# Performance work log

Measured on AMD Instinct MI355X. Metric: run time of the kernel, lower is better.

The kernel has to match this reference:

```python
import jax, jax.numpy as jnp
import numpy as np

RC = 5.0  # cosine cutoff radius

def ssp(z):
    # shifted softplus, SchNet activation
    return jax.nn.softplus(z) - jnp.log(2.0).astype(z.dtype)

def setup_inputs():
    key = jax.random.key(0)
    ks = jax.random.split(key, 16)
    B, Na, Nn, G, F = 2, 2048, 48, 50, 128
    e = jax.random.normal(ks[0], (B, Na, 1), jnp.float32)
    x = jax.random.normal(ks[1], (B, Na, F), jnp.float32)
    t = jax.random.normal(ks[2], (B, Na, 1), jnp.float32)
    r_ij = jax.random.uniform(ks[3], (B, Na, Nn), jnp.float32) * 6.0  # some beyond cutoff
    neighbors = jax.random.randint(ks[4], (B, Na, Nn), 0, Na)
    pairwise_mask = jax.random.randint(ks[5], (B, Na, Nn), 0, 2).astype(jnp.int32)
    f_ij = jax.random.normal(ks[6], (B, Na, Nn, G), jnp.float32)
    def lin(k, fan_in, fan_out):
        return jax.random.normal(k, (fan_in, fan_out), jnp.float32) / np.sqrt(fan_in).astype(np.float32)
    Wf1 = lin(ks[7], G, F); bf1 = jnp.zeros((F,), jnp.float32)
    Wf2 = lin(ks[8], F, F); bf2 = jnp.zeros((F,), jnp.float32)
    Wq = lin(ks[9], F, F)
    Wk = lin(ks[10], F, F)
    Wv = lin(ks[11], F, F)
    Wo = lin(ks[12], F, F); bo = jnp.zeros((F,), jnp.float32)
    return dict(e=e, x=x, t=t, r_ij=r_ij, neighbors=neighbors, pairwise_mask=pairwise_mask,
                f_ij=f_ij, Wf1=Wf1, bf1=bf1, Wf2=Wf2, bf2=bf2, Wq=Wq, Wk=Wk, Wv=Wv, Wo=Wo, bo=bo)

def reference(e, x, t, r_ij, neighbors, pairwise_mask, f_ij,
              Wf1, bf1, Wf2, bf2, Wq, Wk, Wv, Wo, bo):
    B, Na, Nn = neighbors.shape
    F = x.shape[-1]
    # continuous filter from expanded distances: W = filter_network(2*f_ij - 1)
    W = 2.0 * f_ij - 1.0
    W = ssp(W @ Wf1 + bf1) @ Wf2 + bf2                # [B,Na,Nn,F]
    # cosine cutoff
    C = (0.5 * (jnp.cos(jnp.pi * r_ij / RC) + 1.0) * (r_ij < RC))[..., None]  # [B,Na,Nn,1]
    W = W * C
    # gather neighbor embeddings: y[b,i,n,:] = x[b, neighbors[b,i,n], :]
    idx = neighbors.reshape(B, Na * Nn)
    y = jnp.take_along_axis(x, idx[..., None], axis=1).reshape(B, Na, Nn, F)
    y_full = jnp.concatenate([x[:, :, None, :], y], axis=2)  # [B,Na,Nn+1,F] self + neighbors
    # cutoff-masked attention aggregation
    q = x @ Wq                                        # [B,Na,F]
    k = y_full @ Wk                                   # [B,Na,Nn+1,F]
    v = y_full @ Wv
    v = jnp.concatenate([v[:, :, :1, :], v[:, :, 1:, :] * W], axis=2)  # filter-modulated values
    scores = jnp.einsum('baf,banf->ban', q, k) / jnp.sqrt(jnp.float32(F))
    mask = jnp.concatenate([jnp.ones((B, Na, 1), bool), pairwise_mask.astype(bool)], axis=2)
    scores = jnp.where(mask, scores, jnp.float32(-1e9))
    attn = jax.nn.softmax(scores, axis=-1)
    m = jnp.einsum('ban,banf->baf', attn, v)
    m = ssp(m @ Wo + bo)                              # [B,Na,F]
    return (m, W)
```

## Files before the change

### kernel.cpp

```cpp
#include <hip/hip_runtime.h>

typedef unsigned int uint;
typedef unsigned short ushort;

#define B_  2
#define NA  2048
#define NN  48
#define G_  50
#define F_  128
#define NK  49
#define NROW (B_ * NA * NN)
#define NAT  (B_ * NA)

typedef short short8 __attribute__((ext_vector_type(8)));
typedef float floatx4 __attribute__((ext_vector_type(4)));

__device__ __forceinline__ float ssp(float z) {
  return fmaxf(z, 0.f) + __logf(1.f + __expf(-fabsf(z))) - 0.69314718055994531f;
}
__device__ __forceinline__ ushort f2bf(float x) {
  union { float f; uint u; } v; v.f = x;
  uint u = v.u;
  u += 0x7fffu + ((u >> 16) & 1u);
  return (ushort)(u >> 16);
}
__device__ __forceinline__ uint pk2bf(float x, float y) {
  return (uint)f2bf(x) | ((uint)f2bf(y) << 16);
}

extern "C" __global__ __launch_bounds__(256)
void prep_kernel(const float* __restrict__ Wf1, const float* __restrict__ Wf2,
                 const float* __restrict__ Wv, const float* __restrict__ Wo,
                 ushort* __restrict__ Wf1t, ushort* __restrict__ Wf2t,
                 ushort* __restrict__ Wvt, ushort* __restrict__ Wot)
{
  int gid = blockIdx.x * 256 + threadIdx.x;
  if (gid < 8192) {
    int n = gid >> 6, k = gid & 63;
    Wf1t[gid] = f2bf((k < G_) ? Wf1[(size_t)k * F_ + n] : 0.f);
  }
  for (int idx = gid; idx < 3 * 16384; idx += 24576) {
    int m = idx >> 14, e = idx & 16383;
    int n = e >> 7, k = e & 127;
    const float* src = (m == 0) ? Wf2 : (m == 1) ? Wv : Wo;
    ushort* dst = (m == 0) ? Wf2t : (m == 1) ? Wvt : Wot;
    dst[e] = f2bf(src[(size_t)k * F_ + n]);
  }
}

extern "C" __global__ __launch_bounds__(256, 4)
void qk_kernel(const float* __restrict__ x,
               const float* __restrict__ Wq, const float* __restrict__ Wk,
               float* __restrict__ Qo, float* __restrict__ Ko)
{
  __shared__ float xs[32 * 128];
  const int t = threadIdx.x;
  const int f = t & 127, h = t >> 7;
  const size_t Rb = (size_t)blockIdx.x * 32;
  const float* W = blockIdx.y ? Wk : Wq;
  float* O = blockIdx.y ? Ko : Qo;

  {
    const float4* src = (const float4*)(x + Rb * F_);
    float4* dst = (float4*)xs;
    #pragma unroll
    for (int k = 0; k < 4; ++k) dst[t + 256 * k] = src[t + 256 * k];
  }
  __syncthreads();

  float acc[16];
  #pragma unroll
  for (int j = 0; j < 16; ++j) acc[j] = 0.f;
  #pragma unroll
  for (int kc = 0; kc < 4; ++kc) {
    float wr[32];
    #pragma unroll
    for (int kk = 0; kk < 32; ++kk) wr[kk] = W[(size_t)(kc * 32 + kk) * F_ + f];
    #pragma unroll
    for (int j = 0; j < 16; ++j) {
      const float4* xr = (const float4*)&xs[(h * 16 + j) * 128 + kc * 32];
      #pragma unroll
      for (int qq = 0; qq < 8; ++qq) {
        float4 v = xr[qq];
        acc[j] += v.x * wr[qq * 4] + v.y * wr[qq * 4 + 1]
                + v.z * wr[qq * 4 + 2] + v.w * wr[qq * 4 + 3];
      }
    }
  }
  #pragma unroll
  for (int j = 0; j < 16; ++j)
    O[(Rb + h * 16 + j) * F_ + f] = acc[j];
}

extern "C" __global__ __launch_bounds__(256, 4)
void v_kernel(const float* __restrict__ x, const ushort* __restrict__ Wvt,
              float* __restrict__ Vo)
{
  __shared__ ushort xb[16 * 136];
  const int t = threadIdx.x;
  const int lane = t & 63, w = t >> 6;
  const int c16 = lane & 15, q = lane >> 4;
  const size_t Rb = (size_t)blockIdx.x * 16;

  {
    int row = t >> 4, col = (t & 15) * 8;
    float4 v0 = *(const float4*)(x + (Rb + row) * F_ + col);
    float4 v1 = *(const float4*)(x + (Rb + row) * F_ + col + 4);
    uint4 pk = { pk2bf(v0.x, v0.y), pk2bf(v0.z, v0.w),
                 pk2bf(v1.x, v1.y), pk2bf(v1.z, v1.w) };
    *(uint4*)((char*)xb + row * 272 + col * 2) = pk;
  }
  __syncthreads();

  short8 bx[4];
  const char* ap = (const char*)xb + c16 * 272 + q * 16;
  #pragma unroll
  for (int s = 0; s < 4; ++s) bx[s] = *(const short8*)(ap + s * 64);

  #pragma unroll
  for (int u = 0; u < 2; ++u) {
    int ntile = w * 2 + u;
    const char* bb = (const char*)Wvt + (ntile * 16 + c16) * 256 + q * 16;
    floatx4 acc = {0.f, 0.f, 0.f, 0.f};
    #pragma unroll
    for (int s = 0; s < 4; ++s) {
      short8 wf = *(const short8*)(bb + s * 64);
      acc = __builtin_amdgcn_mfma_f32_16x16x32_bf16(wf, bx[s], acc, 0, 0, 0);
    }
    *(floatx4*)(Vo + (Rb + c16) * F_ + ntile * 16 + q * 4) = acc;
  }
}

struct __align__(16) SmemF2 {
  union {
    ushort ft[128 * 72];
    ushort h1[128 * 136];
  } u;
  float C[128];
};

extern "C" __global__ __launch_bounds__(256, 4)
void filter_kernel(const float* __restrict__ fij, const float* __restrict__ r_ij,
                   const ushort* __restrict__ Wf1t, const float* __restrict__ bf1,
                   const ushort* __restrict__ Wf2t, const float* __restrict__ bf2p,
                   float* __restrict__ out_W)
{
  __shared__ SmemF2 sm;
  const int t = threadIdx.x;
  const int lane = t & 63, w = t >> 6;
  const int c16 = lane & 15, q = lane >> 4;
  const int m0 = w * 32;
  const size_t Rb = (size_t)blockIdx.x * 128;

  #pragma unroll
  for (int it = 0; it < 16; ++it) {
    int idx = t + it * 256;
    int row = idx >> 5, kp = idx & 31;
    uint pk = 0;
    if (kp < 25) {
      float2 v = *(const float2*)(fij + (Rb + row) * G_ + 2 * kp);
      pk = pk2bf(2.f * v.x - 1.f, 2.f * v.y - 1.f);
    }
    ((uint*)sm.u.ft)[row * 36 + kp] = pk;
  }
  if (t < 128) {
    float r = r_ij[Rb + t];
    sm.C[t] = (r < 5.0f) ? 0.5f * (cosf(0.62831853071795864769f * r) + 1.0f) : 0.0f;
  }
  __syncthreads();

  short8 a1[2][2];
  #pragma unroll
  for (int mt = 0; mt < 2; ++mt) {
    const char* ap = (const char*)sm.u.ft + (m0 + mt * 16 + c16) * 144 + q * 16;
    a1[mt][0] = *(const short8*)(ap);
    a1[mt][1] = *(const short8*)(ap + 64);
  }
  __syncthreads();

  short8 b1[8][2];
  #pragma unroll
  for (int nt = 0; nt < 8; ++nt) {
    const char* bb = (const char*)Wf1t + (nt * 16 + c16) * 128 + q * 16;
    b1[nt][0] = *(const short8*)(bb);
    b1[nt][1] = *(const short8*)(bb + 64);
  }

  #pragma unroll
  for (int nt = 0; nt < 8; ++nt) {
    int n = nt * 16 + c16;
    float bias = bf1[n];
    #pragma unroll
    for (int mt = 0; mt < 2; ++mt) {
      floatx4 acc = {0.f, 0.f, 0.f, 0.f};
      acc = __builtin_amdgcn_mfma_f32_16x16x32_bf16(a1[mt][0], b1[nt][0], acc, 0, 0, 0);
      acc = __builtin_amdgcn_mfma_f32_16x16x32_bf16(a1[mt][1], b1[nt][1], acc, 0, 0, 0);
      #pragma unroll
      for (int r = 0; r < 4; ++r) {
        int row = m0 + mt * 16 + q * 4 + r;
        sm.u.h1[row * 136 + n] = f2bf(ssp(acc[r] + bias));
      }
    }
  }

  short8 a2[2][4];
  #pragma unroll
  for (int mt = 0; mt < 2; ++mt) {
    const char* ap = (const char*)sm.u.h1 + (m0 + mt * 16 + c16) * 272 + q * 16;
    #pragma unroll
    for (int s = 0; s < 4; ++s) a2[mt][s] = *(const short8*)(ap + s * 64);
  }

  #pragma unroll
  for (int g = 0; g < 2; ++g) {
    short8 b2[4][4];
    #pragma unroll
    for (int j = 0; j < 4; ++j) {
      int n = (g * 4 + j) * 16 + c16;
      const char* bb = (const char*)Wf2t + n * 256 + q * 16;
      #pragma unroll
      for (int s = 0; s < 4; ++s) b2[j][s] = *(const short8*)(bb + s * 64);
    }
    #pragma unroll
    for (int j = 0; j < 4; ++j) {
      int n = (g * 4 + j) * 16 + c16;
      float bias = bf2p[n];
      #pragma unroll
      for (int mt = 0; mt < 2; ++mt) {
        floatx4 acc = {0.f, 0.f, 0.f, 0.f};
        #pragma unroll
        for (int s = 0; s < 4; ++s)
          acc = __builtin_amdgcn_mfma_f32_16x16x32_bf16(a2[mt][s], b2[j][s], acc, 0, 0, 0);
        #pragma unroll
        for (int r = 0; r < 4; ++r) {
          int row = m0 + mt * 16 + q * 4 + r;
          out_W[(Rb + row) * F_ + n] = (acc[r] + bias) * sm.C[row];
        }
      }
    }
  }
}

extern "C" __global__ __launch_bounds__(256, 4)
void attn_kernel(const float* __restrict__ Q, const float* __restrict__ K,
                 const float* __restrict__ V, const float* __restrict__ Wg,
                 const int* __restrict__ nbr, const int* __restrict__ pmask,
                 float* __restrict__ m_pre)
{
  __shared__ float qs[4][128];
  __shared__ float attn_s[4][64];
  __shared__ int   src_s[4][64];
  const int t = threadIdx.x;
  const int lane = t & 63, w = t >> 6;
  const int a = blockIdx.x * 4 + w;
  const int b = a >> 11, i = a & 2047;
  const size_t base_nn = (size_t)a * NN;

  {
    float2 q2 = *(const float2*)(Q + (size_t)a * F_ + lane * 2);
    *(float2*)&qs[w][lane * 2] = q2;
  }

  int src = i;
  int pm = 1;
  if (lane >= 1 && lane <= NN) {
    src = nbr[base_nn + lane - 1];
    pm  = pmask[base_nn + lane - 1];
  }
  src_s[w][lane] = src;

  float s = 0.f;
  const float* Krow = K + ((size_t)b * NA + src) * F_;
  #pragma unroll 8
  for (int c = 0; c < 32; ++c) {
    float4 k4 = *(const float4*)(Krow + c * 4);
    float4 q4 = *(const float4*)&qs[w][c * 4];
    s += q4.x * k4.x + q4.y * k4.y + q4.z * k4.z + q4.w * k4.w;
  }
  s *= 0.08838834764831845f;
  if (lane >= 1 && pm == 0) s = -1e9f;
  if (lane >= NK) s = -1e30f;

  float mx = s;
  #pragma unroll
  for (int o = 32; o; o >>= 1) mx = fmaxf(mx, __shfl_xor(mx, o));
  float ev = (lane < NK) ? __expf(s - mx) : 0.f;
  float sum = ev;
  #pragma unroll
  for (int o = 32; o; o >>= 1) sum += __shfl_xor(sum, o);
  attn_s[w][lane] = ev / sum;

  float2 acc = {0.f, 0.f};
  #pragma unroll 8
  for (int n = 0; n < NK; ++n) {
    float an = attn_s[w][n];
    int   sr = src_s[w][n];
    float2 v2 = *(const float2*)(V + ((size_t)b * NA + sr) * F_ + lane * 2);
    float2 w2 = {1.f, 1.f};
    if (n > 0) w2 = *(const float2*)(Wg + (base_nn + n - 1) * F_ + lane * 2);
    acc.x += an * w2.x * v2.x;
    acc.y += an * w2.y * v2.y;
  }
  *(float2*)(m_pre + (size_t)a * F_ + lane * 2) = acc;
}

extern "C" __global__ __launch_bounds__(256, 4)
void out_kernel(const float* __restrict__ m_pre, const ushort* __restrict__ Wot,
                const float* __restrict__ bo, float* __restrict__ out_m)
{
  __shared__ ushort xb[16 * 136];
  const int t = threadIdx.x;
  const int lane = t & 63, w = t >> 6;
  const int c16 = lane & 15, q = lane >> 4;
  const size_t Rb = (size_t)blockIdx.x * 16;

  {
    int row = t >> 4, col = (t & 15) * 8;
    float4 v0 = *(const float4*)(m_pre + (Rb + row) * F_ + col);
    float4 v1 = *(const float4*)(m_pre + (Rb + row) * F_ + col + 4);
    uint4 pk = { pk2bf(v0.x, v0.y), pk2bf(v0.z, v0.w),
                 pk2bf(v1.x, v1.y), pk2bf(v1.z, v1.w) };
    *(uint4*)((char*)xb + row * 272 + col * 2) = pk;
  }
  __syncthreads();

  short8 bx[4];
  const char* ap = (const char*)xb + c16 * 272 + q * 16;
  #pragma unroll
  for (int s = 0; s < 4; ++s) bx[s] = *(const short8*)(ap + s * 64);

  #pragma unroll
  for (int u = 0; u < 2; ++u) {
    int ntile = w * 2 + u;
    const char* bb = (const char*)Wot + (ntile * 16 + c16) * 256 + q * 16;
    floatx4 acc = {0.f, 0.f, 0.f, 0.f};
    #pragma unroll
    for (int s = 0; s < 4; ++s) {
      short8 wf = *(const short8*)(bb + s * 64);
      acc = __builtin_amdgcn_mfma_f32_16x16x32_bf16(wf, bx[s], acc, 0, 0, 0);
    }
    int n0 = ntile * 16 + q * 4;
    float4 bv = *(const float4*)&bo[n0];
    floatx4 outv;
    outv[0] = ssp(acc[0] + bv.x);
    outv[1] = ssp(acc[1] + bv.y);
    outv[2] = ssp(acc[2] + bv.z);
    outv[3] = ssp(acc[3] + bv.w);
    *(floatx4*)(out_m + (Rb + c16) * F_ + n0) = outv;
  }
}

extern "C" void kernel_launch(void* const* d_in, const int* in_sizes, int n_in,
                              void* d_out, int out_size, void* d_ws, size_t ws_size,
                              hipStream_t stream) {
  const float* x   = (const float*)d_in[1];
  const float* r   = (const float*)d_in[3];
  const int*  nbr  = (const int*)d_in[4];
  const int*  pmk  = (const int*)d_in[5];
  const float* fij = (const float*)d_in[6];
  const float* Wf1 = (const float*)d_in[7];
  const float* bf1 = (const float*)d_in[8];
  const float* Wf2 = (const float*)d_in[9];
  const float* bf2p= (const float*)d_in[10];
  const float* Wq  = (const float*)d_in[11];
  const float* Wk  = (const float*)d_in[12];
  const float* Wv  = (const float*)d_in[13];
  const float* Wo  = (const float*)d_in[14];
  const float* bo  = (const float*)d_in[15];
  float* out_m = (float*)d_out;
  float* out_W = out_m + (size_t)NAT * F_;

  float* Qs = (float*)d_ws;
  float* Ks = Qs + (size_t)NAT * F_;
  float* Vs = Ks + (size_t)NAT * F_;
  float* Ms = Vs + (size_t)NAT * F_;
  ushort* Wf1t = (ushort*)(Ms + (size_t)NAT * F_);
  ushort* Wf2t = Wf1t + 128 * 64;
  ushort* Wvt  = Wf2t + 128 * 128;
  ushort* Wot  = Wvt  + 128 * 128;

  hipLaunchKernelGGL(prep_kernel, dim3(96), dim3(256), 0, stream,
                     Wf1, Wf2, Wv, Wo, Wf1t, Wf2t, Wvt, Wot);
  hipLaunchKernelGGL(qk_kernel, dim3(NAT / 32, 2), dim3(256), 0, stream,
                     x, Wq, Wk, Qs, Ks);
  hipLaunchKernelGGL(v_kernel, dim3(NAT / 16), dim3(256), 0, stream,
                     x, Wvt, Vs);
  hipLaunchKernelGGL(filter_kernel, dim3(NROW / 128), dim3(256), 0, stream,
                     fij, r, Wf1t, bf1, Wf2t, bf2p, out_W);
  hipLaunchKernelGGL(attn_kernel, dim3(NAT / 4), dim3(256), 0, stream,
                     Qs, Ks, Vs, out_W, nbr, pmk, Ms);
  hipLaunchKernelGGL(out_kernel, dim3(NAT / 16), dim3(256), 0, stream,
                     Ms, Wot, bo, out_m);
}
```

Before: 273.2 us.

## Coalesce K loads in attention via per-neighbor warp reductions and batch V/W loads

The attention kernel used to compute scores with each lane reading an entire 512-byte K row on its own, which gives uncoalesced, strided global access. It now processes neighbors one at a time, with the whole wavefront reading one K row as contiguous float2 values and reducing the dot product through xor shuffles. Neighbor indices, mask bits and attention weights are broadcast with shuffles, so the shared-memory arrays are gone. The aggregation loop issues V and W loads in batches of 8 to raise memory-level parallelism. The cost is many more cross-lane shuffle reductions: 49 dot products, each needing a 6-step reduction.

```diff
diff --git a/kernel.cpp b/kernel.cpp
--- a/kernel.cpp
+++ b/kernel.cpp
@@ -247,59 +247,62 @@
                  const int* __restrict__ nbr, const int* __restrict__ pmask,
                  float* __restrict__ m_pre)
 {
-  __shared__ float qs[4][128];
-  __shared__ float attn_s[4][64];
-  __shared__ int   src_s[4][64];
   const int t = threadIdx.x;
   const int lane = t & 63, w = t >> 6;
   const int a = blockIdx.x * 4 + w;
   const int b = a >> 11, i = a & 2047;
   const size_t base_nn = (size_t)a * NN;
 
+  int nbrv = (lane < NN) ? nbr[base_nn + lane] : 0;
+  int pmv  = (lane < NN) ? pmask[base_nn + lane] : 1;
+
+  float2 q2 = *(const float2*)(Q + (size_t)a * F_ + lane * 2);
+
+  float s_lane = -1e30f;
+  #pragma unroll
+  for (int n = 0; n < NK; ++n) {
+    int src = (n == 0) ? i : __shfl(nbrv, (n > 0) ? n - 1 : 0);
+    float2 k2 = *(const float2*)(K + ((size_t)b * NA + src) * F_ + lane * 2);
+    float p = q2.x * k2.x + q2.y * k2.y;
+    #pragma unroll
+    for (int o = 32; o; o >>= 1) p += __shfl_xor(p, o);
+    p *= 0.08838834764831845f;
+    if (n > 0 && __shfl(pmv, n - 1) == 0) p = -1e9f;
+    if (lane == n) s_lane = p;
+  }
+
+  float mx = s_lane;
+  #pragma unroll
+  for (int o = 32; o; o >>= 1) mx = fmaxf(mx, __shfl_xor(mx, o));
+  float ev = (lane < NK) ? __expf(s_lane - mx) : 0.f;
+  float sum = ev;
+  #pragma unroll
+  for (int o = 32; o; o >>= 1) sum += __shfl_xor(sum, o);
+  float attn_l = ev / sum;
+
+  float2 acc;
   {
-    float2 q2 = *(const float2*)(Q + (size_t)a * F_ + lane * 2);
-    *(float2*)&qs[w][lane * 2] = q2;
-  }
-
-  int src = i;
-  int pm = 1;
-  if (lane >= 1 && lane <= NN) {
-    src = nbr[base_nn + lane - 1];
-    pm  = pmask[base_nn + lane - 1];
-  }
-  src_s[w][lane] = src;
-
-  float s = 0.f;
-  const float* Krow = K + ((size_t)b * NA + src) * F_;
-  #pragma unroll 8
-  for (int c = 0; c < 32; ++c) {
-    float4 k4 = *(const float4*)(Krow + c * 4);
-    float4 q4 = *(const float4*)&qs[w][c * 4];
-    s += q4.x * k4.x + q4.y * k4.y + q4.z * k4.z + q4.w * k4.w;
-  }
-  s *= 0.08838834764831845f;
-  if (lane >= 1 && pm == 0) s = -1e9f;
-  if (lane >= NK) s = -1e30f;
-
-  float mx = s;
-  #pragma unroll
-  for (int o = 32; o; o >>= 1) mx = fmaxf(mx, __shfl_xor(mx, o));
-  float ev = (lane < NK) ? __expf(s - mx) : 0.f;
-  float sum = ev;
-  #pragma unroll
-  for (int o = 32; o; o >>= 1) sum += __shfl_xor(sum, o);
-  attn_s[w][lane] = ev / sum;
-
-  float2 acc = {0.f, 0.f};
-  #pragma unroll 8
-  for (int n = 0; n < NK; ++n) {
-    float an = attn_s[w][n];
-    int   sr = src_s[w][n];
-    float2 v2 = *(const float2*)(V + ((size_t)b * NA + sr) * F_ + lane * 2);
-    float2 w2 = {1.f, 1.f};
-    if (n > 0) w2 = *(const float2*)(Wg + (base_nn + n - 1) * F_ + lane * 2);
-    acc.x += an * w2.x * v2.x;
-    acc.y += an * w2.y * v2.y;
+    float a0 = __shfl(attn_l, 0);
+    float2 vi = *(const float2*)(V + ((size_t)b * NA + i) * F_ + lane * 2);
+    acc.x = a0 * vi.x;
+    acc.y = a0 * vi.y;
+  }
+  for (int c = 0; c < 6; ++c) {
+    float an[8];
+    float2 vv[8], wv[8];
+    #pragma unroll
+    for (int j = 0; j < 8; ++j) {
+      int n = c * 8 + j + 1;
+      an[j] = __shfl(attn_l, n);
+      int sr = __shfl(nbrv, n - 1);
+      vv[j] = *(const float2*)(V + ((size_t)b * NA + sr) * F_ + lane * 2);
+      wv[j] = *(const float2*)(Wg + (base_nn + n - 1) * F_ + lane * 2);
+    }
+    #pragma unroll
+    for (int j = 0; j < 8; ++j) {
+      acc.x += an[j] * wv[j].x * vv[j].x;
+      acc.y += an[j] * wv[j].y * vv[j].y;
+    }
   }
   *(float2*)(m_pre + (size_t)a * F_ + lane * 2) = acc;
 }
```

After: 271.1 us. About the same (-0.8%).
